# Optimization experiments

Measured on AMD Instinct MI355X. Metric: run time of the kernel, lower is better.

## Reference

```python
import jax, jax.numpy as jnp
import numpy as np

N_NODES = 100000
N_EDGES = 3200000
N_FEAT = 128
HIDDEN = 64
N_GRAPHS = 128


def setup_inputs() -> dict:
    key = jax.random.key(0)
    ks = jax.random.split(key, 8)
    x = jax.random.normal(ks[0], (N_NODES, N_FEAT), dtype=jnp.float32)
    edge_index = jax.random.randint(ks[1], (2, N_EDGES), 0, N_NODES, dtype=jnp.int64)
    batch = jnp.sort(jax.random.randint(ks[2], (N_NODES,), 0, N_GRAPHS, dtype=jnp.int64))
    W1 = jax.random.normal(ks[3], (N_FEAT, HIDDEN), dtype=jnp.float32) / np.sqrt(N_FEAT)
    b1 = jnp.zeros((HIDDEN,), dtype=jnp.float32)
    W2 = jax.random.normal(ks[4], (HIDDEN, HIDDEN), dtype=jnp.float32) / np.sqrt(HIDDEN)
    b2 = jnp.zeros((HIDDEN,), dtype=jnp.float32)
    Wlin = jax.random.normal(ks[5], (HIDDEN, 10), dtype=jnp.float32) / np.sqrt(HIDDEN)
    blin = jnp.zeros((10,), dtype=jnp.float32)
    return {"x": x, "edge_index": edge_index, "batch": batch,
            "W1": W1, "b1": b1, "W2": W2, "b2": b2, "Wlin": Wlin, "blin": blin}


def gcn_conv(x, src, dst, W, b, n):
    # PyG GCNConv: A_hat = D^{-1/2}(A+I)D^{-1/2};  out = A_hat @ (x W) + b
    xw = x @ W  # [N, H]
    ones = jnp.ones((src.shape[0],), dtype=xw.dtype)
    deg = jax.ops.segment_sum(ones, dst, num_segments=n) + 1.0  # +1 self-loop
    dinv = jax.lax.rsqrt(deg)  # deg >= 1 always
    norm = dinv[src] * dinv[dst]  # per-edge normalization
    agg = jax.ops.segment_sum(norm[:, None] * xw[src], dst, num_segments=n)
    agg = agg + (dinv * dinv)[:, None] * xw  # self-loop contribution
    return agg + b


def reference(x, edge_index, batch, W1, b1, W2, b2, Wlin, blin):
    src, dst = edge_index[0], edge_index[1]
    n = x.shape[0]
    h = gcn_conv(x, src, dst, W1, b1, n)
    h = jax.nn.relu(h)
    h = gcn_conv(h, src, dst, W2, b2, n)
    # global_mean_pool over batch segment ids
    sums = jax.ops.segment_sum(h, batch, num_segments=N_GRAPHS)
    cnts = jax.ops.segment_sum(jnp.ones((n,), dtype=h.dtype), batch, num_segments=N_GRAPHS)
    pooled = sums / jnp.maximum(cnts, 1.0)[:, None]  # [G, H]
    out = pooled @ Wlin + blin  # [G, 10]
    return out.reshape(-1)
```

## Files before the change

### kernel.cpp

```cpp
#include <hip/hip_runtime.h>
#include <hip/hip_bf16.h>

#define NNODES 100000
#define NEDGES 3200000
#define NFEAT 128
#define HID 64
#define NGRAPHS 128

#define BSHIFT 9
#define BSIZE 512
#define NBUCK_MAX 256
#define EPB 8192
#define GCH 16



__global__ __launch_bounds__(256, 4) void kA_gemm1_hist(
    const float* __restrict__ X, const float* __restrict__ W,
    const int* __restrict__ ei, int* __restrict__ btotal,
    int* __restrict__ blkcnt,
    float* __restrict__ Y, int n, int nE, int nbuck, int nblkh, int nGemm) {
    __shared__ __align__(16) float sXT[64][65];
    __shared__ __align__(16) float sW[64][64];
    __shared__ int cnt[NBUCK_MAX];
    int bid = blockIdx.x;
    int r5 = bid % 5, q5 = bid / 5;
    int t = threadIdx.x;
    if (r5 != 4) {
        int qb = q5 * 4 + r5;
        if (qb >= nGemm) return;
        int brow = qb * 64;
        int row = t >> 2, c0 = (t & 3) << 4;
        float4 a0 = make_float4(0.f, 0.f, 0.f, 0.f);
        float4 a1 = a0, a2 = a0, a3 = a0;
        for (int kt = 0; kt < NFEAT; kt += 64) {
            const float4* X4 = (const float4*)X;
            const int rs = NFEAT >> 2;
#pragma unroll
            for (int j = 0; j < 4; ++j) {
                int idx = t + j * 256;
                int r = idx >> 4, c4 = idx & 15;
                int gr = brow + r;
                float4 v = make_float4(0.f, 0.f, 0.f, 0.f);
                if (gr < n) v = X4[(size_t)gr * rs + (kt >> 2) + c4];
                int c = c4 << 2;
                sXT[c][r] = v.x; sXT[c + 1][r] = v.y;
                sXT[c + 2][r] = v.z; sXT[c + 3][r] = v.w;
            }
            const float4* W4 = (const float4*)W;
#pragma unroll
            for (int j = 0; j < 4; ++j) {
                int idx = t + j * 256;
                int k = idx >> 4, c4 = idx & 15;
                *(float4*)&sW[k][c4 << 2] = W4[(size_t)(kt + k) * 16 + c4];
            }
            __syncthreads();
#pragma unroll 4
            for (int k = 0; k < 64; ++k) {
                float xv = sXT[k][row];
                float4 w0 = *(const float4*)&sW[k][c0];
                float4 w1 = *(const float4*)&sW[k][c0 + 4];
                float4 w2 = *(const float4*)&sW[k][c0 + 8];
                float4 w3 = *(const float4*)&sW[k][c0 + 12];
                a0.x = fmaf(xv, w0.x, a0.x); a0.y = fmaf(xv, w0.y, a0.y);
                a0.z = fmaf(xv, w0.z, a0.z); a0.w = fmaf(xv, w0.w, a0.w);
                a1.x = fmaf(xv, w1.x, a1.x); a1.y = fmaf(xv, w1.y, a1.y);
                a1.z = fmaf(xv, w1.z, a1.z); a1.w = fmaf(xv, w1.w, a1.w);
                a2.x = fmaf(xv, w2.x, a2.x); a2.y = fmaf(xv, w2.y, a2.y);
                a2.z = fmaf(xv, w2.z, a2.z); a2.w = fmaf(xv, w2.w, a2.w);
                a3.x = fmaf(xv, w3.x, a3.x); a3.y = fmaf(xv, w3.y, a3.y);
                a3.z = fmaf(xv, w3.z, a3.z); a3.w = fmaf(xv, w3.w, a3.w);
            }
            __syncthreads();
        }
        int gr = brow + row;
        if (gr < n) {
            float4* Y4 = (float4*)Y;
            size_t base = (size_t)gr * 16 + (c0 >> 2);
            Y4[base + 0] = a0; Y4[base + 1] = a1;
            Y4[base + 2] = a2; Y4[base + 3] = a3;
        }
    } else {
        int h = q5;
        for (int i = t; i < nbuck; i += 256) cnt[i] = 0;
        __syncthreads();
        int base = h * EPB;
        int end = min(base + EPB, nE);
        for (int e = base + t; e < end; e += 256) {
            int d = ei[nE + e];
            atomicAdd(&cnt[d >> BSHIFT], 1);
        }
        __syncthreads();
        for (int i = t; i < nbuck; i += 256) {
            int c = cnt[i];
            blkcnt[(size_t)i * nblkh + h] = c;
            if (c) atomicAdd(&btotal[i], c);
        }
    }
}


__global__ __launch_bounds__(256) void k_boff(const int* __restrict__ btotal,
                                              const int* __restrict__ blkcnt,
                                              int* __restrict__ blkoff,
                                              int* __restrict__ bbase_g, int nblkh) {
    __shared__ int vals[256];
    __shared__ int row[512];
    int b = blockIdx.x, t = threadIdx.x;
    vals[t] = (t < b) ? btotal[t] : 0;
    __syncthreads();
    for (int off = 128; off > 0; off >>= 1) {
        if (t < off) vals[t] += vals[t + off];
        __syncthreads();
    }
    int bbase = vals[0];
    for (int i = t; i < nblkh; i += 256) row[i] = blkcnt[(size_t)b * nblkh + i];
    __syncthreads();
    if (t == 0) {
        bbase_g[b] = bbase;
        int run = bbase;
        for (int i = 0; i < nblkh; ++i) { int x = row[i]; row[i] = run; run += x; }
    }
    __syncthreads();
    for (int i = t; i < nblkh; i += 256) blkoff[(size_t)b * nblkh + i] = row[i];
}


__global__ __launch_bounds__(256) void kC_scatter(const int* __restrict__ ei,
                                                  const int* __restrict__ blkoff,
                                                  int* __restrict__ bucketed,
                                                  int nE, int nbuck, int nblkh) {
    __shared__ int gcur[NBUCK_MAX];
    int h = blockIdx.x, t = threadIdx.x;
    for (int i = t; i < nbuck; i += 256) gcur[i] = blkoff[(size_t)i * nblkh + h];
    __syncthreads();
    int base = h * EPB;
    int end = min(base + EPB, nE);
    for (int e = base + t; e < end; e += 256) {
        int s = ei[e];
        int d = ei[nE + e];
        int b = d >> BSHIFT, dl = d & (BSIZE - 1);
        int pos = atomicAdd(&gcur[b], 1);
        bucketed[pos] = s | (dl << 17);
    }
}


__global__ __launch_bounds__(256) void kD_sort(const int* __restrict__ bucketed,
                                               const int* __restrict__ btotal,
                                               const int* __restrict__ bbase_g,
                                               int* __restrict__ ptr,
                                               float* __restrict__ dinv,
                                               int* __restrict__ csrc,
                                               int n, int nE, int nbuck) {
    __shared__ int hist[BSIZE];
    __shared__ int cur[BSIZE];
    int b = blockIdx.x, t = threadIdx.x;
    int bbase = bbase_g[b];
    int esz = btotal[b];
    int n0 = b << BSHIFT;
    int nn = min(BSIZE, n - n0);
    for (int i = t; i < BSIZE; i += 256) hist[i] = 0;
    __syncthreads();
    for (int k = t; k < esz; k += 256)
        atomicAdd(&hist[bucketed[bbase + k] >> 17], 1);
    __syncthreads();
    for (int i = t; i < nn; i += 256)
        dinv[n0 + i] = 1.0f / sqrtf((float)hist[i] + 1.0f);
    __syncthreads();
    if (t == 0) {
        int run = 0;
        for (int i = 0; i < nn; ++i) { int x = hist[i]; hist[i] = run; run += x; }
    }
    __syncthreads();
    for (int i = t; i < nn; i += 256) {
        ptr[n0 + i] = bbase + hist[i];
        cur[i] = hist[i];
    }
    if (b == nbuck - 1 && t == 0) ptr[n] = nE;
    __syncthreads();
    for (int k = t; k < esz; k += 256) {
        int p = bucketed[bbase + k];
        int dl = p >> 17, src = p & 0x1FFFF;
        int r = atomicAdd(&cur[dl], 1);
        csrc[bbase + r] = src;
    }
}


__global__ void k_cnt(const int* __restrict__ batch, int* __restrict__ gcnt, int n) {
    __shared__ int h[NGRAPHS];
    int t = threadIdx.x;
    if (t < NGRAPHS) h[t] = 0;
    __syncthreads();
    int base = blockIdx.x * 1024;
    int end = min(base + 1024, n);
    for (int i = base + t; i < end; i += 256) atomicAdd(&h[batch[i]], 1);
    __syncthreads();
    if (t < NGRAPHS && h[t]) atomicAdd(&gcnt[t], h[t]);
}

__global__ void k_ginv(const int* __restrict__ gcnt, float* __restrict__ ginv) {
    int t = threadIdx.x;
    if (t < NGRAPHS) ginv[t] = 1.f / fmaxf((float)gcnt[t], 1.f);
}

__global__ void k_wc(const float* __restrict__ W2, const float* __restrict__ Wlin,
                     const float* __restrict__ b2, const float* __restrict__ blin,
                     float* __restrict__ Wc, float* __restrict__ bc) {
    int t = threadIdx.x;
    for (int idx = t; idx < 64 * 16; idx += 256) {
        int k = idx >> 4, c = idx & 15;
        float a = 0.f;
        if (c < 10) {
#pragma unroll 8
            for (int m = 0; m < 64; ++m) a = fmaf(W2[k * 64 + m], Wlin[m * 10 + c], a);
        }
        Wc[idx] = a;
    }
    if (t < 16) {
        float a = 0.f;
        if (t < 10) {
            a = blin[t];
            for (int m = 0; m < 64; ++m) a = fmaf(b2[m], Wlin[m * 10 + t], a);
        }
        bc[t] = a;
    }
}


__global__ __launch_bounds__(256) void k_g1mm(const float4* __restrict__ Y1,
                                              const int* __restrict__ ptr,
                                              const int* __restrict__ csrc,
                                              const float* __restrict__ dinv,
                                              const float4* __restrict__ b1_4,
                                              const float* __restrict__ Wc,
                                              float* __restrict__ rbuf, int n) {
    __shared__ float sWc[64][17];
    __shared__ float hrow[4][64];
    {
        int t = threadIdx.x;
#pragma unroll
        for (int j = 0; j < 4; ++j) {
            int idx = t + j * 256;
            sWc[idx >> 4][idx & 15] = Wc[idx];
        }
    }
    int wv = threadIdx.x >> 6, lane = threadIdx.x & 63;
    int q = lane >> 4, f4 = lane & 15;
    int node = blockIdx.x * 4 + wv;
    bool act = node < n;
    float di = 0.f;
    if (act) {
        int s = ptr[node], e = ptr[node + 1];
        float4 acc = make_float4(0.f, 0.f, 0.f, 0.f);
        int k = s + q;
        while (k + 4 < e) {
            int s0 = csrc[k], s1 = csrc[k + 4];
            float d0 = dinv[s0], d1 = dinv[s1];
            float4 v0 = Y1[(size_t)s0 * 16 + f4];
            float4 v1 = Y1[(size_t)s1 * 16 + f4];
            acc.x += v0.x * d0 + v1.x * d1;
            acc.y += v0.y * d0 + v1.y * d1;
            acc.z += v0.z * d0 + v1.z * d1;
            acc.w += v0.w * d0 + v1.w * d1;
            k += 8;
        }
        if (k < e) {
            int s0 = csrc[k];
            float d0 = dinv[s0];
            float4 v0 = Y1[(size_t)s0 * 16 + f4];
            acc.x += v0.x * d0; acc.y += v0.y * d0;
            acc.z += v0.z * d0; acc.w += v0.w * d0;
        }
#pragma unroll
        for (int m = 16; m <= 32; m <<= 1) {
            acc.x += __shfl_xor(acc.x, m);
            acc.y += __shfl_xor(acc.y, m);
            acc.z += __shfl_xor(acc.z, m);
            acc.w += __shfl_xor(acc.w, m);
        }
        di = dinv[node];
        float4 self = Y1[(size_t)node * 16 + f4];
        float4 b = b1_4[f4];
        float4 h;
        h.x = fmaxf(fmaf(di, fmaf(di, self.x, acc.x), b.x), 0.f);
        h.y = fmaxf(fmaf(di, fmaf(di, self.y, acc.y), b.y), 0.f);
        h.z = fmaxf(fmaf(di, fmaf(di, self.z, acc.z), b.z), 0.f);
        h.w = fmaxf(fmaf(di, fmaf(di, self.w, acc.w), b.w), 0.f);
        if (q == 0) {
            int c = f4 << 2;
            hrow[wv][c] = h.x; hrow[wv][c + 1] = h.y;
            hrow[wv][c + 2] = h.z; hrow[wv][c + 3] = h.w;
        }
    }
    __syncthreads();
    if (act) {
        float p = 0.f;
        int kb = q << 4;
#pragma unroll
        for (int i = 0; i < 16; ++i)
            p = fmaf(hrow[wv][kb + i], sWc[kb + i][f4], p);
        p += __shfl_xor(p, 16);
        p += __shfl_xor(p, 32);
        if (lane < 16)
            rbuf[(size_t)node * 16 + lane] = di * p;
    }
}


__global__ __launch_bounds__(256) void k_gpool(const float4* __restrict__ rbuf4,
                                               const int* __restrict__ ptr,
                                               const int* __restrict__ csrc,
                                               const float* __restrict__ dinv,
                                               const int* __restrict__ batch,
                                               const float* __restrict__ ginv,
                                               float* __restrict__ gsum, int n) {
    int wave = blockIdx.x * 4 + (threadIdx.x >> 6);
    int lane = threadIdx.x & 63;
    int quad = lane >> 2, f4 = lane & 3;
    int start = wave * GCH;
    if (start >= n) return;
    int end = min(start + GCH, n);
    int g = batch[start];
    float4 gacc = make_float4(0.f, 0.f, 0.f, 0.f);
    for (int nd = start; nd < end; ++nd) {
        int gn = batch[nd];
        if (gn != g) {
            if (quad == 0) {
                atomicAdd(&gsum[g * 16 + f4 * 4 + 0], gacc.x);
                atomicAdd(&gsum[g * 16 + f4 * 4 + 1], gacc.y);
                atomicAdd(&gsum[g * 16 + f4 * 4 + 2], gacc.z);
                atomicAdd(&gsum[g * 16 + f4 * 4 + 3], gacc.w);
            }
            gacc = make_float4(0.f, 0.f, 0.f, 0.f);
            g = gn;
        }
        int s = ptr[nd], e = ptr[nd + 1];
        float4 acc = make_float4(0.f, 0.f, 0.f, 0.f);
        if (quad == 0) acc = rbuf4[(size_t)nd * 4 + f4];
        for (int k = s + quad; k < e; k += 16) {
            float4 v = rbuf4[(size_t)csrc[k] * 4 + f4];
            acc.x += v.x; acc.y += v.y; acc.z += v.z; acc.w += v.w;
        }
#pragma unroll
        for (int m = 4; m <= 32; m <<= 1) {
            acc.x += __shfl_xor(acc.x, m);
            acc.y += __shfl_xor(acc.y, m);
            acc.z += __shfl_xor(acc.z, m);
            acc.w += __shfl_xor(acc.w, m);
        }
        float sc = dinv[nd] * ginv[g];
        if (quad == 0) {
            gacc.x = fmaf(sc, acc.x, gacc.x);
            gacc.y = fmaf(sc, acc.y, gacc.y);
            gacc.z = fmaf(sc, acc.z, gacc.z);
            gacc.w = fmaf(sc, acc.w, gacc.w);
        }
    }
    if (quad == 0) {
        atomicAdd(&gsum[g * 16 + f4 * 4 + 0], gacc.x);
        atomicAdd(&gsum[g * 16 + f4 * 4 + 1], gacc.y);
        atomicAdd(&gsum[g * 16 + f4 * 4 + 2], gacc.z);
        atomicAdd(&gsum[g * 16 + f4 * 4 + 3], gacc.w);
    }
}

__global__ void k_fin2(const float* __restrict__ gsum, const float* __restrict__ bc,
                       float* __restrict__ out) {
    int i = blockIdx.x * 256 + threadIdx.x;
    if (i < NGRAPHS * 10) {
        int g = i / 10, c = i - g * 10;
        out[i] = gsum[g * 16 + c] + bc[c];
    }
}


extern "C" void kernel_launch(void* const* d_in, const int* in_sizes, int n_in,
                              void* d_out, int out_size, void* d_ws, size_t ws_size,
                              hipStream_t stream) {
    const float* x     = (const float*)d_in[0];
    const int*   ei    = (const int*)d_in[1];
    const int*   batch = (const int*)d_in[2];
    const float* W1    = (const float*)d_in[3];
    const float* b1    = (const float*)d_in[4];
    const float* W2    = (const float*)d_in[5];
    const float* b2    = (const float*)d_in[6];
    const float* Wlin  = (const float*)d_in[7];
    const float* blin  = (const float*)d_in[8];
    float* out = (float*)d_out;

    int n  = in_sizes[0] / NFEAT;
    int nE = in_sizes[1] / 2;

    int nbuck = (n + BSIZE - 1) >> BSHIFT;
    int nblkh = (nE + EPB - 1) / EPB;
    int nGemm = (n + 63) / 64;

    char* ws = (char*)d_ws;
    auto alloc = [&](size_t b) -> void* {
        void* p = (void*)ws;
        ws += (b + 255) & ~(size_t)255;
        return p;
    };
    float* dinv    = (float*)alloc((size_t)n * 4);
    int*   ptr     = (int*)alloc((size_t)(n + 1) * 4);
    int*   btotal  = (int*)alloc((size_t)nbuck * 4);
    int*   bbase_g = (int*)alloc((size_t)nbuck * 4);
    int*   blkcnt  = (int*)alloc((size_t)nbuck * nblkh * 4);
    int*   blkoff  = (int*)alloc((size_t)nbuck * nblkh * 4);
    int*   bucketed= (int*)alloc((size_t)nE * 4);
    int*   csrc    = (int*)alloc((size_t)nE * 4);
    float* bufA    = (float*)alloc((size_t)n * HID * 4);
    float* rbuf    = (float*)alloc((size_t)n * 16 * 4);
    int*   gcnt    = (int*)alloc((size_t)NGRAPHS * 4);
    float* ginv    = (float*)alloc((size_t)NGRAPHS * 4);
    float* Wc      = (float*)alloc(64 * 16 * 4);
    float* bc      = (float*)alloc(16 * 4);
    float* gsum    = (float*)alloc((size_t)NGRAPHS * 16 * 4);

    hipMemsetAsync(btotal, 0, (size_t)nbuck * 4, stream);
    hipMemsetAsync(gcnt, 0, (size_t)NGRAPHS * 4, stream);
    hipMemsetAsync(gsum, 0, (size_t)NGRAPHS * 16 * 4, stream);

    kA_gemm1_hist<<<5 * nblkh, 256, 0, stream>>>(x, W1, ei, btotal, blkcnt,
                                                 bufA, n, nE, nbuck, nblkh, nGemm);
    k_boff<<<nbuck, 256, 0, stream>>>(btotal, blkcnt, blkoff, bbase_g, nblkh);
    kC_scatter<<<nblkh, 256, 0, stream>>>(ei, blkoff, bucketed, nE, nbuck, nblkh);
    kD_sort<<<nbuck, 256, 0, stream>>>(bucketed, btotal, bbase_g, ptr, dinv,
                                       csrc, n, nE, nbuck);

    k_cnt<<<(n + 1023) / 1024, 256, 0, stream>>>(batch, gcnt, n);
    k_ginv<<<1, NGRAPHS, 0, stream>>>(gcnt, ginv);
    k_wc<<<1, 256, 0, stream>>>(W2, Wlin, b2, blin, Wc, bc);

    k_g1mm<<<(n + 3) / 4, 256, 0, stream>>>((const float4*)bufA, ptr, csrc, dinv,
                                            (const float4*)b1, Wc, rbuf, n);
    int gwaves = (n + GCH - 1) / GCH;
    k_gpool<<<(gwaves + 3) / 4, 256, 0, stream>>>((const float4*)rbuf, ptr, csrc,
                                                  dinv, batch, ginv, gsum, n);
    k_fin2<<<5, 256, 0, stream>>>(gsum, bc, out);
}
```

Measured before the change: 415.2 us.

## Prescale node features by dinv in sort kernel and unroll gathers four-deep

```diff
diff --git a/kernel.cpp b/kernel.cpp
--- a/kernel.cpp
+++ b/kernel.cpp
@@ -152,9 +152,11 @@
                                                int* __restrict__ ptr,
                                                float* __restrict__ dinv,
                                                int* __restrict__ csrc,
+                                               float* __restrict__ bufA,
                                                int n, int nE, int nbuck) {
     __shared__ int hist[BSIZE];
     __shared__ int cur[BSIZE];
+    __shared__ float sdv[BSIZE];
     int b = blockIdx.x, t = threadIdx.x;
     int bbase = bbase_g[b];
     int esz = btotal[b];
@@ -165,8 +167,11 @@
     for (int k = t; k < esz; k += 256)
         atomicAdd(&hist[bucketed[bbase + k] >> 17], 1);
     __syncthreads();
-    for (int i = t; i < nn; i += 256)
-        dinv[n0 + i] = 1.0f / sqrtf((float)hist[i] + 1.0f);
+    for (int i = t; i < nn; i += 256) {
+        float d = 1.0f / sqrtf((float)hist[i] + 1.0f);
+        dinv[n0 + i] = d;
+        sdv[i] = d;
+    }
     __syncthreads();
     if (t == 0) {
         int run = 0;
@@ -185,6 +190,14 @@
         int r = atomicAdd(&cur[dl], 1);
         csrc[bbase + r] = src;
     }
+    float4* A4 = (float4*)bufA;
+    size_t base4 = (size_t)n0 * 16;
+    for (int i4 = t; i4 < nn * 16; i4 += 256) {
+        float sc = sdv[i4 >> 4];
+        float4 v = A4[base4 + i4];
+        v.x *= sc; v.y *= sc; v.z *= sc; v.w *= sc;
+        A4[base4 + i4] = v;
+    }
 }
 
 
@@ -207,7 +220,8 @@
 
 __global__ void k_wc(const float* __restrict__ W2, const float* __restrict__ Wlin,
                      const float* __restrict__ b2, const float* __restrict__ blin,
-                     float* __restrict__ Wc, float* __restrict__ bc) {
+                     float* __restrict__ Wc, float* __restrict__ bc,
+                     float* __restrict__ zrow) {
     int t = threadIdx.x;
     for (int idx = t; idx < 64 * 16; idx += 256) {
         int k = idx >> 4, c = idx & 15;
@@ -226,6 +240,7 @@
         }
         bc[t] = a;
     }
+    if (t >= 64 && t < 128) zrow[t - 64] = 0.f;
 }
 
 
@@ -235,77 +250,68 @@
                                               const float* __restrict__ dinv,
                                               const float4* __restrict__ b1_4,
                                               const float* __restrict__ Wc,
+                                              const float4* __restrict__ zrow,
                                               float* __restrict__ rbuf, int n) {
     __shared__ float sWc[64][17];
     __shared__ float hrow[4][64];
-    {
-        int t = threadIdx.x;
-#pragma unroll
-        for (int j = 0; j < 4; ++j) {
-            int idx = t + j * 256;
-            sWc[idx >> 4][idx & 15] = Wc[idx];
-        }
-    }
-    int wv = threadIdx.x >> 6, lane = threadIdx.x & 63;
+    int t = threadIdx.x;
+#pragma unroll
+    for (int j = 0; j < 4; ++j) {
+        int idx = t + j * 256;
+        sWc[idx >> 4][idx & 15] = Wc[idx];
+    }
+    __syncthreads();
+    int wv = t >> 6, lane = t & 63;
     int q = lane >> 4, f4 = lane & 15;
     int node = blockIdx.x * 4 + wv;
-    bool act = node < n;
-    float di = 0.f;
-    if (act) {
-        int s = ptr[node], e = ptr[node + 1];
-        float4 acc = make_float4(0.f, 0.f, 0.f, 0.f);
-        int k = s + q;
-        while (k + 4 < e) {
-            int s0 = csrc[k], s1 = csrc[k + 4];
-            float d0 = dinv[s0], d1 = dinv[s1];
-            float4 v0 = Y1[(size_t)s0 * 16 + f4];
-            float4 v1 = Y1[(size_t)s1 * 16 + f4];
-            acc.x += v0.x * d0 + v1.x * d1;
-            acc.y += v0.y * d0 + v1.y * d1;
-            acc.z += v0.z * d0 + v1.z * d1;
-            acc.w += v0.w * d0 + v1.w * d1;
-            k += 8;
-        }
-        if (k < e) {
-            int s0 = csrc[k];
-            float d0 = dinv[s0];
-            float4 v0 = Y1[(size_t)s0 * 16 + f4];
-            acc.x += v0.x * d0; acc.y += v0.y * d0;
-            acc.z += v0.z * d0; acc.w += v0.w * d0;
-        }
-#pragma unroll
-        for (int m = 16; m <= 32; m <<= 1) {
-            acc.x += __shfl_xor(acc.x, m);
-            acc.y += __shfl_xor(acc.y, m);
-            acc.z += __shfl_xor(acc.z, m);
-            acc.w += __shfl_xor(acc.w, m);
-        }
-        di = dinv[node];
-        float4 self = Y1[(size_t)node * 16 + f4];
-        float4 b = b1_4[f4];
-        float4 h;
-        h.x = fmaxf(fmaf(di, fmaf(di, self.x, acc.x), b.x), 0.f);
-        h.y = fmaxf(fmaf(di, fmaf(di, self.y, acc.y), b.y), 0.f);
-        h.z = fmaxf(fmaf(di, fmaf(di, self.z, acc.z), b.z), 0.f);
-        h.w = fmaxf(fmaf(di, fmaf(di, self.w, acc.w), b.w), 0.f);
-        if (q == 0) {
-            int c = f4 << 2;
-            hrow[wv][c] = h.x; hrow[wv][c + 1] = h.y;
-            hrow[wv][c + 2] = h.z; hrow[wv][c + 3] = h.w;
-        }
-    }
-    __syncthreads();
-    if (act) {
-        float p = 0.f;
-        int kb = q << 4;
-#pragma unroll
-        for (int i = 0; i < 16; ++i)
-            p = fmaf(hrow[wv][kb + i], sWc[kb + i][f4], p);
-        p += __shfl_xor(p, 16);
-        p += __shfl_xor(p, 32);
-        if (lane < 16)
-            rbuf[(size_t)node * 16 + lane] = di * p;
-    }
+    if (node >= n) return;
+    int s = ptr[node], e = ptr[node + 1];
+    float di = dinv[node];
+    float4 self = Y1[(size_t)node * 16 + f4];
+    float4 acc = make_float4(0.f, 0.f, 0.f, 0.f);
+    for (int k = s + q; k < e; k += 16) {
+        int k1 = k + 4, k2 = k + 8, k3 = k + 12;
+        int s0 = csrc[k];
+        int s1 = (k1 < e) ? csrc[k1] : -1;
+        int s2 = (k2 < e) ? csrc[k2] : -1;
+        int s3 = (k3 < e) ? csrc[k3] : -1;
+        const float4* p0 = Y1 + (size_t)s0 * 16;
+        const float4* p1 = (s1 >= 0) ? Y1 + (size_t)s1 * 16 : zrow;
+        const float4* p2 = (s2 >= 0) ? Y1 + (size_t)s2 * 16 : zrow;
+        const float4* p3 = (s3 >= 0) ? Y1 + (size_t)s3 * 16 : zrow;
+        float4 v0 = p0[f4], v1 = p1[f4], v2 = p2[f4], v3 = p3[f4];
+        acc.x += (v0.x + v1.x) + (v2.x + v3.x);
+        acc.y += (v0.y + v1.y) + (v2.y + v3.y);
+        acc.z += (v0.z + v1.z) + (v2.z + v3.z);
+        acc.w += (v0.w + v1.w) + (v2.w + v3.w);
+    }
+#pragma unroll
+    for (int m = 16; m <= 32; m <<= 1) {
+        acc.x += __shfl_xor(acc.x, m);
+        acc.y += __shfl_xor(acc.y, m);
+        acc.z += __shfl_xor(acc.z, m);
+        acc.w += __shfl_xor(acc.w, m);
+    }
+    float4 b = b1_4[f4];
+    float4 h;
+    h.x = fmaxf(fmaf(di, acc.x + self.x, b.x), 0.f);
+    h.y = fmaxf(fmaf(di, acc.y + self.y, b.y), 0.f);
+    h.z = fmaxf(fmaf(di, acc.z + self.z, b.z), 0.f);
+    h.w = fmaxf(fmaf(di, acc.w + self.w, b.w), 0.f);
+    if (q == 0) {
+        int c = f4 << 2;
+        hrow[wv][c] = h.x; hrow[wv][c + 1] = h.y;
+        hrow[wv][c + 2] = h.z; hrow[wv][c + 3] = h.w;
+    }
+    float p = 0.f;
+    int kb = q << 4;
+#pragma unroll
+    for (int i = 0; i < 16; ++i)
+        p = fmaf(hrow[wv][kb + i], sWc[kb + i][f4], p);
+    p += __shfl_xor(p, 16);
+    p += __shfl_xor(p, 32);
+    if (lane < 16)
+        rbuf[(size_t)node * 16 + lane] = di * p;
 }
 
 
@@ -315,6 +321,7 @@
                                                const float* __restrict__ dinv,
                                                const int* __restrict__ batch,
                                                const float* __restrict__ ginv,
+                                               const float4* __restrict__ zrow4,
                                                float* __restrict__ gsum, int n) {
     int wave = blockIdx.x * 4 + (threadIdx.x >> 6);
     int lane = threadIdx.x & 63;
@@ -339,9 +346,17 @@
         int s = ptr[nd], e = ptr[nd + 1];
         float4 acc = make_float4(0.f, 0.f, 0.f, 0.f);
         if (quad == 0) acc = rbuf4[(size_t)nd * 4 + f4];
-        for (int k = s + quad; k < e; k += 16) {
-            float4 v = rbuf4[(size_t)csrc[k] * 4 + f4];
-            acc.x += v.x; acc.y += v.y; acc.z += v.z; acc.w += v.w;
+        for (int k = s + quad; k < e; k += 64) {
+            int k1 = k + 16, k2 = k + 32, k3 = k + 48;
+            const float4* p0 = rbuf4 + (size_t)csrc[k] * 4;
+            const float4* p1 = (k1 < e) ? rbuf4 + (size_t)csrc[k1] * 4 : zrow4;
+            const float4* p2 = (k2 < e) ? rbuf4 + (size_t)csrc[k2] * 4 : zrow4;
+            const float4* p3 = (k3 < e) ? rbuf4 + (size_t)csrc[k3] * 4 : zrow4;
+            float4 v0 = p0[f4], v1 = p1[f4], v2 = p2[f4], v3 = p3[f4];
+            acc.x += (v0.x + v1.x) + (v2.x + v3.x);
+            acc.y += (v0.y + v1.y) + (v2.y + v3.y);
+            acc.z += (v0.z + v1.z) + (v2.z + v3.z);
+            acc.w += (v0.w + v1.w) + (v2.w + v3.w);
         }
 #pragma unroll
         for (int m = 4; m <= 32; m <<= 1) {
@@ -417,6 +432,7 @@
     float* ginv    = (float*)alloc((size_t)NGRAPHS * 4);
     float* Wc      = (float*)alloc(64 * 16 * 4);
     float* bc      = (float*)alloc(16 * 4);
+    float* zrow    = (float*)alloc(64 * 4);
     float* gsum    = (float*)alloc((size_t)NGRAPHS * 16 * 4);
 
     hipMemsetAsync(btotal, 0, (size_t)nbuck * 4, stream);
@@ -428,16 +444,18 @@
     k_boff<<<nbuck, 256, 0, stream>>>(btotal, blkcnt, blkoff, bbase_g, nblkh);
     kC_scatter<<<nblkh, 256, 0, stream>>>(ei, blkoff, bucketed, nE, nbuck, nblkh);
     kD_sort<<<nbuck, 256, 0, stream>>>(bucketed, btotal, bbase_g, ptr, dinv,
-                                       csrc, n, nE, nbuck);
+                                       csrc, bufA, n, nE, nbuck);
 
     k_cnt<<<(n + 1023) / 1024, 256, 0, stream>>>(batch, gcnt, n);
     k_ginv<<<1, NGRAPHS, 0, stream>>>(gcnt, ginv);
-    k_wc<<<1, 256, 0, stream>>>(W2, Wlin, b2, blin, Wc, bc);
+    k_wc<<<1, 256, 0, stream>>>(W2, Wlin, b2, blin, Wc, bc, zrow);
 
     k_g1mm<<<(n + 3) / 4, 256, 0, stream>>>((const float4*)bufA, ptr, csrc, dinv,
-                                            (const float4*)b1, Wc, rbuf, n);
+                                            (const float4*)b1, Wc,
+                                            (const float4*)zrow, rbuf, n);
     int gwaves = (n + GCH - 1) / GCH;
     k_gpool<<<(gwaves + 3) / 4, 256, 0, stream>>>((const float4*)rbuf, ptr, csrc,
-                                                  dinv, batch, ginv, gsum, n);
+                                                  dinv, batch, ginv,
+                                                  (const float4*)zrow, gsum, n);
     k_fin2<<<5, 256, 0, stream>>>(gsum, bc, out);
 }
```

Result: no change. 411.4 us (-0.9%).
